# Kernel tuning notes

Hardware: AMD Instinct MI355X
Metric: run time of the kernel (lower is better)

Reference implementation:

```python
import jax, jax.numpy as jnp
import numpy as np

EMB = 128
BINS = 32
CUT = 5.0
NLAYER = 5
NHID = 4  # extra hidden linears in edge MLP (hidden_dim_list has 5 entries total)
N_NODES = 50000
N_EDGES = 800000
N_GRAPH = 256
NODE_CLASS = 100


def setup_inputs() -> dict:
    key = jax.random.key(0)
    ks = jax.random.split(key, 20)
    s = 0.02
    inp = {
        'z': jax.random.randint(ks[0], (N_NODES,), 0, NODE_CLASS),
        'pos': jax.random.normal(ks[1], (N_NODES, 3), dtype=jnp.float32) * 3.0,
        'batch': jnp.sort(jax.random.randint(ks[2], (N_NODES,), 0, N_GRAPH)),
        'edge_index': jax.random.randint(ks[3], (2, N_EDGES), 0, N_NODES),
        # parameters
        'atom_table': jax.random.normal(ks[4], (NODE_CLASS, EMB), dtype=jnp.float32) * s,
        'atom_w': jax.random.normal(ks[5], (EMB, EMB), dtype=jnp.float32) * s,
        'atom_b': jnp.zeros((EMB,), jnp.float32),
        'edge_emb_w': jax.random.normal(ks[6], (BINS, EMB), dtype=jnp.float32) * s,
        'edge_emb_b': jnp.zeros((EMB,), jnp.float32),
        'edge_w0': jax.random.normal(ks[7], (NLAYER, 3 * EMB, EMB), dtype=jnp.float32) * s,
        'edge_b0': jnp.zeros((NLAYER, EMB), jnp.float32),
        'edge_w': jax.random.normal(ks[8], (NLAYER, NHID, EMB, EMB), dtype=jnp.float32) * s,
        'edge_b': jnp.zeros((NLAYER, NHID, EMB), jnp.float32),
        'node_w': jax.random.normal(ks[9], (NLAYER, EMB, EMB), dtype=jnp.float32) * s,
        'node_b': jnp.zeros((NLAYER, EMB), jnp.float32),
        'out_w': jax.random.normal(ks[10], (EMB, 1), dtype=jnp.float32) * s,
        'out_b': jnp.zeros((1,), jnp.float32),
    }
    return inp


def reference(z, pos, batch, edge_index, atom_table, atom_w, atom_b,
              edge_emb_w, edge_emb_b, edge_w0, edge_b0, edge_w, edge_b,
              node_w, node_b, out_w, out_b):
    silu = jax.nn.silu
    row, col = edge_index[0], edge_index[1]

    # atom embedding + linear
    h_node = atom_table[z] @ atom_w + atom_b  # [N, EMB]

    # edge distances -> gaussian basis expansion (linear spacing, log_base=1.0)
    d = jnp.linalg.norm(pos[row] - pos[col], axis=-1)  # [E]
    mu = jnp.linspace(0.0, CUT, BINS, dtype=jnp.float32)
    sigma = CUT / BINS
    basis = jnp.exp(-0.5 * ((d[:, None] - mu) / sigma) ** 2)  # [E, BINS]
    h_edge = basis @ edge_emb_w + edge_emb_b  # [E, EMB]

    # message passing layers
    for l in range(NLAYER):
        m = jnp.concatenate([h_edge, h_node[row], h_node[col]], axis=-1)  # [E, 3*EMB]
        m = silu(m @ edge_w0[l] + edge_b0[l])
        for k in range(NHID):
            m = silu(m @ edge_w[l, k] + edge_b[l, k])
        h_edge = h_edge + m  # residual edge update
        agg = jax.ops.segment_sum(h_edge, row, num_segments=N_NODES)  # [N, EMB]
        h_node = h_node + silu(agg @ node_w[l] + node_b[l])  # residual node update

    # scatter-mean graph pool
    sums = jax.ops.segment_sum(h_node, batch, num_segments=N_GRAPH)
    cnt = jax.ops.segment_sum(jnp.ones((h_node.shape[0],), h_node.dtype), batch, num_segments=N_GRAPH)
    h_graph = sums / jnp.clip(cnt, 1.0)[:, None]

    return h_graph @ out_w + out_b  # [N_GRAPH, 1]
```

## Files before the change

### kernel.cpp

```cpp
#include <hip/hip_runtime.h>

#define EMB      128
#define N_NODES_ 50000
#define N_EDGES_ 800000
#define N_GRAPH_ 256
#define NLAYER_  5

#define WP_ATOM  573440
#define WP_NODE0 589824
#define WP_EMB   671744
#define WP_TOTAL 675840

typedef short short8 __attribute__((ext_vector_type(8)));
typedef float floatx4 __attribute__((ext_vector_type(4)));

__device__ __forceinline__ float silu_f(float x) {
    return __fdividef(x, 1.0f + __expf(-x));
}
__device__ __forceinline__ float bf2f(unsigned short h) {
    return __uint_as_float(((unsigned)h) << 16);
}
__device__ __forceinline__ unsigned short f2bf(float f) {
    unsigned u = __float_as_uint(f);
    unsigned r = 0x7FFFu + ((u >> 16) & 1u);
    return (unsigned short)((u + r) >> 16);
}

#if defined(__has_builtin)
#if __has_builtin(__builtin_amdgcn_cvt_pk_bf16_f32)
#define HAVE_PK_BF16 1
#endif
#endif
#ifdef HAVE_PK_BF16
typedef __bf16 bf16x2 __attribute__((ext_vector_type(2)));
__device__ __forceinline__ unsigned f2bf_pk(float a, float b) {
    bf16x2 v = __builtin_amdgcn_cvt_pk_bf16_f32(a, b);
    unsigned u;
    __builtin_memcpy(&u, &v, 4);
    return u;
}
#else
__device__ __forceinline__ unsigned f2bf_pk(float a, float b) {
    return (unsigned)f2bf(a) | ((unsigned)f2bf(b) << 16);
}
#endif

__device__ __forceinline__ void wave_lds_fence() {
    __builtin_amdgcn_fence(__ATOMIC_ACQ_REL, "wavefront");
    __builtin_amdgcn_wave_barrier();
}

__device__ __forceinline__ void gload_lds16(const unsigned short* g, unsigned short* l) {
    __builtin_amdgcn_global_load_lds(
        (const __attribute__((address_space(1))) void*)g,
        (__attribute__((address_space(3))) void*)l,
        16, 0, 0);
}

__global__ __launch_bounds__(256) void hist_kernel(
    const int* __restrict__ row, int* __restrict__ hist)
{
    const int e = blockIdx.x * 256 + threadIdx.x;
    if (e < N_EDGES_) atomicAdd(&hist[row[e]], 1);
}

__global__ __launch_bounds__(256) void scan_kernel(
    const int* __restrict__ hist, int* __restrict__ cursor)
{
    __shared__ int ssum[256];
    const int tid = threadIdx.x;
    const int chunk = (N_NODES_ + 255) / 256;
    const int base = tid * chunk;
    int s = 0;
    for (int i = 0; i < chunk; ++i) {
        const int idx = base + i;
        if (idx < N_NODES_) s += hist[idx];
    }
    ssum[tid] = s;
    __syncthreads();
    for (int off = 1; off < 256; off <<= 1) {
        const int t2 = (tid >= off) ? ssum[tid - off] : 0;
        __syncthreads();
        ssum[tid] += t2;
        __syncthreads();
    }
    int run = ssum[tid] - s;
    for (int i = 0; i < chunk; ++i) {
        const int idx = base + i;
        if (idx < N_NODES_) { cursor[idx] = run; run += hist[idx]; }
    }
}

__global__ __launch_bounds__(256) void scatter_kernel(
    const int* __restrict__ row, const int* __restrict__ col,
    int* __restrict__ cursor, int* __restrict__ row_s, int* __restrict__ col_s)
{
    const int e = blockIdx.x * 256 + threadIdx.x;
    if (e >= N_EDGES_) return;
    const int r = row[e];
    const int p = atomicAdd(&cursor[r], 1);
    row_s[p] = r;
    col_s[p] = col[e];
}

__global__ __launch_bounds__(256) void pack_w_kernel(
    const float* __restrict__ edge_w0, const float* __restrict__ edge_w,
    const float* __restrict__ atom_w, const float* __restrict__ node_w,
    const float* __restrict__ edge_emb_w,
    unsigned short* __restrict__ Wp)
{
    const int bid = blockIdx.x;
    int Kb, t;
    const float* src;
    unsigned short* dst;
    if (bid < 200) {
        const int l = bid / 40, r = bid % 40, s = r / 8;
        t = r % 8;
        Kb = (s == 0) ? 12 : 4;
        src = (s == 0) ? edge_w0 + (size_t)l * 384 * 128
                       : edge_w + ((size_t)l * 4 + (s - 1)) * 128 * 128;
        dst = Wp + (size_t)l * 114688 + ((s == 0) ? 0 : (49152 + (s - 1) * 16384))
            + (size_t)t * Kb * 512;
    } else if (bid < 208) {
        t = bid - 200; Kb = 4; src = atom_w;
        dst = Wp + WP_ATOM + (size_t)t * Kb * 512;
    } else if (bid < 248) {
        const int l = (bid - 208) >> 3; t = (bid - 208) & 7; Kb = 4;
        src = node_w + (size_t)l * 128 * 128;
        dst = Wp + WP_NODE0 + (size_t)l * 16384 + (size_t)t * Kb * 512;
    } else {
        t = bid - 248; Kb = 1; src = edge_emb_w;
        dst = Wp + WP_EMB + (size_t)t * 512;
    }
    const int n = Kb * 512;
    for (int p = threadIdx.x; p < n; p += 256) {
        const int j = p & 7, lane = (p >> 3) & 63, kb = p >> 9;
        const int k  = kb * 32 + ((lane >> 4) << 3) + j;
        const int nn = t * 16 + (lane & 15);
        dst[p] = f2bf(src[(size_t)k * 128 + nn]);
    }
}

__global__ __launch_bounds__(256, 4) void u_gemm_kernel(
    const unsigned short* __restrict__ h_node_bf,
    const unsigned short* __restrict__ Wp0, const float* __restrict__ b0,
    unsigned short* __restrict__ Ur, unsigned short* __restrict__ Uc, int N)
{
    __shared__ __align__(16) unsigned short B[64][136];
    const int tid  = threadIdx.x;
    const int lane = tid & 63;
    const int wv   = tid >> 6;
    const int n0   = blockIdx.x * 64;

    {
        const int t = tid >> 2, q = tid & 3;
        const int node = n0 + t;
#pragma unroll
        for (int i = 0; i < 4; ++i) {
            const int k8 = (q + 4 * i) << 3;
            short8 v = (short8){0,0,0,0,0,0,0,0};
            if (node < N) v = *(const short8*)&h_node_bf[(size_t)node * 128 + k8];
            *(short8*)&B[t][k8] = v;
        }
    }
    wave_lds_fence();

    const int lr = lane & 15, lg = lane >> 4;
    floatx4 accr[8], accc[8];
#pragma unroll
    for (int nt = 0; nt < 8; ++nt) {
        const float4 bv = *(const float4*)&b0[nt * 16 + lg * 4];
        accr[nt] = (floatx4){bv.x, bv.y, bv.z, bv.w};
        accc[nt] = (floatx4){0.f, 0.f, 0.f, 0.f};
    }
    const unsigned short* brow = &B[wv * 16 + lr][0];
#pragma unroll 2
    for (int kb = 0; kb < 4; ++kb) {
        const short8 mf = *(const short8*)(brow + kb * 32 + lg * 8);
#pragma unroll
        for (int nt = 0; nt < 8; ++nt) {
            const short8 wr = *(const short8*)(Wp0 + ((size_t)(nt * 12 + 4 + kb) * 64 + lane) * 8);
            const short8 wc = *(const short8*)(Wp0 + ((size_t)(nt * 12 + 8 + kb) * 64 + lane) * 8);
            accr[nt] = __builtin_amdgcn_mfma_f32_16x16x32_bf16(wr, mf, accr[nt], 0, 0, 0);
            accc[nt] = __builtin_amdgcn_mfma_f32_16x16x32_bf16(wc, mf, accc[nt], 0, 0, 0);
        }
    }
    const int node = n0 + wv * 16 + lr;
    if (node < N) {
        unsigned short* rrow = Ur + (size_t)node * 128;
        unsigned short* crow = Uc + (size_t)node * 128;
#pragma unroll
        for (int nt = 0; nt < 8; ++nt) {
            uint2 o;
            o.x = f2bf_pk(accr[nt][0], accr[nt][1]);
            o.y = f2bf_pk(accr[nt][2], accr[nt][3]);
            *(uint2*)(rrow + nt * 16 + lg * 4) = o;
            o.x = f2bf_pk(accc[nt][0], accc[nt][1]);
            o.y = f2bf_pk(accc[nt][2], accc[nt][3]);
            *(uint2*)(crow + nt * 16 + lg * 4) = o;
        }
    }
}

__global__ __launch_bounds__(256, 5) void edge_mlp_csr_kernel(
    const unsigned short* __restrict__ h_edge,
    const unsigned short* __restrict__ Ur, const unsigned short* __restrict__ Uc,
    const int* __restrict__ row_s, const int* __restrict__ col_s,
    const unsigned short* __restrict__ Wp, const float* __restrict__ bh)
{
    __shared__ __align__(16) unsigned short Xs[8192];
    __shared__ __align__(16) unsigned short Ys[8192];

    const int tid  = threadIdx.x;
    const int e0   = blockIdx.x * 64;
    const int lane = tid & 63;
    const int wv   = tid >> 6;
    const int lr   = lane & 15;
    const int lg   = lane >> 4;
    const int nt0  = 2 * wv, nt1 = nt0 + 1;

    int rid[4], cid[4];
#pragma unroll
    for (int et = 0; et < 4; ++et) {
        const int e = e0 + et * 16 + lr;
        rid[et] = row_s[e];
        cid[et] = col_s[e];
    }

    const int srow = 16 * wv + lg;
#pragma unroll
    for (int j = 0; j < 4; ++j) {
        const int r = srow + 4 * j;
        const int c = lr ^ (r & 7);
        gload_lds16(h_edge + (size_t)(e0 + r) * 128 + c * 8,
                    &Xs[(16 * wv + 4 * j) * 128]);
    }

    uint2 gr0[4], gr1[4], gc0[4], gc1[4];
#pragma unroll
    for (int et = 0; et < 4; ++et) {
        gr0[et] = *(const uint2*)(Ur + (size_t)rid[et] * 128 + nt0 * 16 + lg * 4);
        gr1[et] = *(const uint2*)(Ur + (size_t)rid[et] * 128 + nt1 * 16 + lg * 4);
        gc0[et] = *(const uint2*)(Uc + (size_t)cid[et] * 128 + nt0 * 16 + lg * 4);
        gc1[et] = *(const uint2*)(Uc + (size_t)cid[et] * 128 + nt1 * 16 + lg * 4);
    }

    asm volatile("s_waitcnt vmcnt(0)" ::: "memory");
    __syncthreads();

    floatx4 acc0[4], acc1[4];
#pragma unroll
    for (int et = 0; et < 4; ++et) {
        acc0[et][0] = bf2f((unsigned short)(gr0[et].x & 0xFFFF)) + bf2f((unsigned short)(gc0[et].x & 0xFFFF));
        acc0[et][1] = bf2f((unsigned short)(gr0[et].x >> 16))    + bf2f((unsigned short)(gc0[et].x >> 16));
        acc0[et][2] = bf2f((unsigned short)(gr0[et].y & 0xFFFF)) + bf2f((unsigned short)(gc0[et].y & 0xFFFF));
        acc0[et][3] = bf2f((unsigned short)(gr0[et].y >> 16))    + bf2f((unsigned short)(gc0[et].y >> 16));
        acc1[et][0] = bf2f((unsigned short)(gr1[et].x & 0xFFFF)) + bf2f((unsigned short)(gc1[et].x & 0xFFFF));
        acc1[et][1] = bf2f((unsigned short)(gr1[et].x >> 16))    + bf2f((unsigned short)(gc1[et].x >> 16));
        acc1[et][2] = bf2f((unsigned short)(gr1[et].y & 0xFFFF)) + bf2f((unsigned short)(gc1[et].y & 0xFFFF));
        acc1[et][3] = bf2f((unsigned short)(gr1[et].y >> 16))    + bf2f((unsigned short)(gc1[et].y >> 16));
    }

    const unsigned short* aptr0 = Wp + ((size_t)(nt0 * 12) * 64 + lane) * 8;
    const unsigned short* aptr1 = Wp + ((size_t)(nt1 * 12) * 64 + lane) * 8;
#pragma unroll 2
    for (int kk = 0; kk < 4; ++kk) {
        const short8 wf0 = *(const short8*)(aptr0 + (size_t)kk * 512);
        const short8 wf1 = *(const short8*)(aptr1 + (size_t)kk * 512);
#pragma unroll
        for (int et = 0; et < 4; ++et) {
            const int r = et * 16 + lr;
            const short8 mf = *(const short8*)&Xs[r * 128 + (((kk * 4 + lg) ^ (r & 7)) << 3)];
            acc0[et] = __builtin_amdgcn_mfma_f32_16x16x32_bf16(wf0, mf, acc0[et], 0, 0, 0);
            acc1[et] = __builtin_amdgcn_mfma_f32_16x16x32_bf16(wf1, mf, acc1[et], 0, 0, 0);
        }
    }

    const int t_ = tid >> 2, q_ = tid & 3;
    short8 he_reg[4];
#pragma unroll
    for (int i = 0; i < 4; ++i) {
        const int ch = q_ + 4 * i;
        he_reg[i] = *(const short8*)&Xs[t_ * 128 + ((ch ^ (t_ & 7)) << 3)];
    }

#pragma unroll
    for (int et = 0; et < 4; ++et) {
        const int r = et * 16 + lr;
        uint2 p0, p1;
        p0.x = f2bf_pk(silu_f(acc0[et][0]), silu_f(acc0[et][1]));
        p0.y = f2bf_pk(silu_f(acc0[et][2]), silu_f(acc0[et][3]));
        p1.x = f2bf_pk(silu_f(acc1[et][0]), silu_f(acc1[et][1]));
        p1.y = f2bf_pk(silu_f(acc1[et][2]), silu_f(acc1[et][3]));
        const int c0 = (2 * nt0 + (lg >> 1)) ^ (r & 7);
        const int c1 = (2 * nt1 + (lg >> 1)) ^ (r & 7);
        *(uint2*)&Ys[r * 128 + c0 * 8 + (lg & 1) * 4] = p0;
        *(uint2*)&Ys[r * 128 + c1 * 8 + (lg & 1) * 4] = p1;
    }
    __syncthreads();

#pragma unroll 1
    for (int s = 1; s < 5; ++s) {
        const unsigned short* bin = (s & 1) ? Ys : Xs;
        unsigned short* bout      = (s & 1) ? Xs : Ys;
        const unsigned short* __restrict__ Ws = Wp + 49152 + (size_t)(s - 1) * 16384;
        const float* __restrict__ bias = bh + (size_t)(s - 1) * 128;

        const float4 bv0 = *(const float4*)&bias[nt0 * 16 + lg * 4];
        const float4 bv1 = *(const float4*)&bias[nt1 * 16 + lg * 4];
#pragma unroll
        for (int et = 0; et < 4; ++et) {
            acc0[et] = (floatx4){bv0.x, bv0.y, bv0.z, bv0.w};
            acc1[et] = (floatx4){bv1.x, bv1.y, bv1.z, bv1.w};
        }
        const unsigned short* ap0 = Ws + ((size_t)(nt0 * 4) * 64 + lane) * 8;
        const unsigned short* ap1 = Ws + ((size_t)(nt1 * 4) * 64 + lane) * 8;
#pragma unroll 2
        for (int kk = 0; kk < 4; ++kk) {
            const short8 wf0 = *(const short8*)(ap0 + (size_t)kk * 512);
            const short8 wf1 = *(const short8*)(ap1 + (size_t)kk * 512);
#pragma unroll
            for (int et = 0; et < 4; ++et) {
                const int r = et * 16 + lr;
                const short8 mf = *(const short8*)&bin[r * 128 + (((kk * 4 + lg) ^ (r & 7)) << 3)];
                acc0[et] = __builtin_amdgcn_mfma_f32_16x16x32_bf16(wf0, mf, acc0[et], 0, 0, 0);
                acc1[et] = __builtin_amdgcn_mfma_f32_16x16x32_bf16(wf1, mf, acc1[et], 0, 0, 0);
            }
        }
#pragma unroll
        for (int et = 0; et < 4; ++et) {
            const int r = et * 16 + lr;
            uint2 p0, p1;
            p0.x = f2bf_pk(silu_f(acc0[et][0]), silu_f(acc0[et][1]));
            p0.y = f2bf_pk(silu_f(acc0[et][2]), silu_f(acc0[et][3]));
            p1.x = f2bf_pk(silu_f(acc1[et][0]), silu_f(acc1[et][1]));
            p1.y = f2bf_pk(silu_f(acc1[et][2]), silu_f(acc1[et][3]));
            const int c0 = (2 * nt0 + (lg >> 1)) ^ (r & 7);
            const int c1 = (2 * nt1 + (lg >> 1)) ^ (r & 7);
            *(uint2*)&bout[r * 128 + c0 * 8 + (lg & 1) * 4] = p0;
            *(uint2*)&bout[r * 128 + c1 * 8 + (lg & 1) * 4] = p1;
        }
        __syncthreads();
    }

#pragma unroll
    for (int i = 0; i < 4; ++i) {
        const int ch = q_ + 4 * i;
        const short8 mv = *(const short8*)&Ys[t_ * 128 + ((ch ^ (t_ & 7)) << 3)];
        const short8 ov = he_reg[i];
        float he[8];
#pragma unroll
        for (int j = 0; j < 8; ++j)
            he[j] = bf2f((unsigned short)ov[j]) + bf2f((unsigned short)mv[j]);
        uint4 sv;
        sv.x = f2bf_pk(he[0], he[1]);
        sv.y = f2bf_pk(he[2], he[3]);
        sv.z = f2bf_pk(he[4], he[5]);
        sv.w = f2bf_pk(he[6], he[7]);
        *(uint4*)(const_cast<unsigned short*>(h_edge) + (size_t)(e0 + t_) * 128 + ch * 8) = sv;
    }
}

__global__ __launch_bounds__(256, 4) void node_agg_gemm_kernel(
    const unsigned short* __restrict__ h_edge,
    const int* __restrict__ hist, const int* __restrict__ cur_end,
    const unsigned short* __restrict__ Wpm, const float* __restrict__ bias,
    unsigned short* __restrict__ h_node_bf, int N)
{
    __shared__ __align__(16) unsigned short B[64][136];
    const int tid  = threadIdx.x;
    const int lane = tid & 63;
    const int wv   = tid >> 6;
    const int n0   = blockIdx.x * 64;

    {
        const int t = tid >> 2, q = tid & 3;
        const int n = n0 + t;
        float a[32];
#pragma unroll
        for (int j = 0; j < 32; ++j) a[j] = 0.f;
        if (n < N) {
            const int e_end = cur_end[n];
            const int e_beg = e_end - hist[n];
            for (int e = e_beg; e < e_end; ++e) {
                const unsigned short* p = &h_edge[(size_t)e * 128 + q * 32];
#pragma unroll
                for (int g = 0; g < 4; ++g) {
                    const short8 v = *(const short8*)(p + g * 8);
#pragma unroll
                    for (int j = 0; j < 8; ++j)
                        a[g * 8 + j] += bf2f((unsigned short)v[j]);
                }
            }
        }
#pragma unroll
        for (int g = 0; g < 4; ++g) {
            uint4 pk;
            pk.x = f2bf_pk(a[g * 8 + 0], a[g * 8 + 1]);
            pk.y = f2bf_pk(a[g * 8 + 2], a[g * 8 + 3]);
            pk.z = f2bf_pk(a[g * 8 + 4], a[g * 8 + 5]);
            pk.w = f2bf_pk(a[g * 8 + 6], a[g * 8 + 7]);
            *(uint4*)&B[t][q * 32 + g * 8] = pk;
        }
    }
    wave_lds_fence();

    const int lr = lane & 15, lg = lane >> 4;
    floatx4 acc[8];
#pragma unroll
    for (int nt = 0; nt < 8; ++nt) {
        const float4 bv = *(const float4*)&bias[nt * 16 + lg * 4];
        acc[nt] = (floatx4){bv.x, bv.y, bv.z, bv.w};
    }
    const unsigned short* brow = &B[wv * 16 + lr][0];
#pragma unroll 2
    for (int kb = 0; kb < 4; ++kb) {
        const short8 mf = *(const short8*)(brow + kb * 32 + lg * 8);
#pragma unroll
        for (int nt = 0; nt < 8; ++nt) {
            const short8 wf = *(const short8*)(Wpm + ((size_t)(nt * 4 + kb) * 64 + lane) * 8);
            acc[nt] = __builtin_amdgcn_mfma_f32_16x16x32_bf16(wf, mf, acc[nt], 0, 0, 0);
        }
    }
    const int node = n0 + wv * 16 + lr;
    if (node < N) {
        unsigned short* drow = &h_node_bf[(size_t)node * 128];
#pragma unroll
        for (int nt = 0; nt < 8; ++nt) {
            float x0 = silu_f(acc[nt][0]), x1 = silu_f(acc[nt][1]);
            float x2 = silu_f(acc[nt][2]), x3 = silu_f(acc[nt][3]);
            unsigned short* p = drow + nt * 16 + lg * 4;
            const uint2 d = *(const uint2*)p;
            x0 += bf2f((unsigned short)(d.x & 0xFFFF));
            x1 += bf2f((unsigned short)(d.x >> 16));
            x2 += bf2f((unsigned short)(d.y & 0xFFFF));
            x3 += bf2f((unsigned short)(d.y >> 16));
            uint2 o;
            o.x = f2bf_pk(x0, x1);
            o.y = f2bf_pk(x2, x3);
            *(uint2*)p = o;
        }
    }
}

__global__ __launch_bounds__(256, 4) void atom_gemm_mfma_kernel(
    const float* __restrict__ src, const int* __restrict__ gidx,
    const unsigned short* __restrict__ Wpm, const float* __restrict__ bias,
    unsigned short* __restrict__ dst, int N)
{
    __shared__ __align__(16) unsigned short B[64][136];
    const int tid  = threadIdx.x;
    const int lane = tid & 63;
    const int wv   = tid >> 6;
    const int n0   = blockIdx.x * 64;

    {
        const int t = tid >> 2, q = tid & 3;
        const int node = n0 + t;
        const float* srow = src;
        if (node < N) srow = &src[(size_t)gidx[node] * 128];
#pragma unroll
        for (int i = 0; i < 4; ++i) {
            const int k8 = (q + 4 * i) << 3;
            uint4 pk = make_uint4(0, 0, 0, 0);
            if (node < N) {
                const float4 f0 = *(const float4*)(srow + k8);
                const float4 f1 = *(const float4*)(srow + k8 + 4);
                pk.x = f2bf_pk(f0.x, f0.y);
                pk.y = f2bf_pk(f0.z, f0.w);
                pk.z = f2bf_pk(f1.x, f1.y);
                pk.w = f2bf_pk(f1.z, f1.w);
            }
            *(uint4*)&B[t][k8] = pk;
        }
    }
    wave_lds_fence();

    const int lr = lane & 15, lg = lane >> 4;
    floatx4 acc[8];
#pragma unroll
    for (int nt = 0; nt < 8; ++nt) {
        const float4 bv = *(const float4*)&bias[nt * 16 + lg * 4];
        acc[nt] = (floatx4){bv.x, bv.y, bv.z, bv.w};
    }
    const unsigned short* brow = &B[wv * 16 + lr][0];
#pragma unroll 2
    for (int kb = 0; kb < 4; ++kb) {
        const short8 mf = *(const short8*)(brow + kb * 32 + lg * 8);
#pragma unroll
        for (int nt = 0; nt < 8; ++nt) {
            const short8 wf = *(const short8*)(Wpm + ((size_t)(nt * 4 + kb) * 64 + lane) * 8);
            acc[nt] = __builtin_amdgcn_mfma_f32_16x16x32_bf16(wf, mf, acc[nt], 0, 0, 0);
        }
    }
    const int node = n0 + wv * 16 + lr;
    if (node < N) {
        unsigned short* drow = &dst[(size_t)node * 128];
#pragma unroll
        for (int nt = 0; nt < 8; ++nt) {
            uint2 o;
            o.x = f2bf_pk(acc[nt][0], acc[nt][1]);
            o.y = f2bf_pk(acc[nt][2], acc[nt][3]);
            *(uint2*)(drow + nt * 16 + lg * 4) = o;
        }
    }
}

__global__ __launch_bounds__(256, 4) void edge_embed_mfma_kernel(
    const float* __restrict__ pos, const int* __restrict__ row, const int* __restrict__ col,
    const unsigned short* __restrict__ Wpe, const float* __restrict__ bemb,
    unsigned short* __restrict__ h_edge)
{
    __shared__ __align__(16) unsigned short Bas[64][40];
    const int tid  = threadIdx.x;
    const int lane = tid & 63;
    const int wv   = tid >> 6;
    const int e0   = blockIdx.x * 64;

    {
        const int t = tid >> 2, q = tid & 3;
        const int rr = row[e0 + t], cc = col[e0 + t];
        const float dx = pos[rr * 3 + 0] - pos[cc * 3 + 0];
        const float dy = pos[rr * 3 + 1] - pos[cc * 3 + 1];
        const float dz = pos[rr * 3 + 2] - pos[cc * 3 + 2];
        const float d = sqrtf(dx * dx + dy * dy + dz * dz);
        const float invs = 32.0f / 5.0f;
        float e[8];
#pragma unroll
        for (int j = 0; j < 8; ++j) {
            const float mu = (float)(q * 8 + j) * (5.0f / 31.0f);
            const float tt = (d - mu) * invs;
            e[j] = __expf(-0.5f * tt * tt);
        }
        uint4 pk;
        pk.x = f2bf_pk(e[0], e[1]);
        pk.y = f2bf_pk(e[2], e[3]);
        pk.z = f2bf_pk(e[4], e[5]);
        pk.w = f2bf_pk(e[6], e[7]);
        *(uint4*)&Bas[t][q * 8] = pk;
    }
    wave_lds_fence();

    const int lr = lane & 15, lg = lane >> 4;
    floatx4 acc[8];
#pragma unroll
    for (int nt = 0; nt < 8; ++nt) {
        const float4 bv = *(const float4*)&bemb[nt * 16 + lg * 4];
        acc[nt] = (floatx4){bv.x, bv.y, bv.z, bv.w};
    }
    const short8 mf = *(const short8*)&Bas[wv * 16 + lr][lg * 8];
#pragma unroll
    for (int nt = 0; nt < 8; ++nt) {
        const short8 wf = *(const short8*)(Wpe + ((size_t)nt * 64 + lane) * 8);
        acc[nt] = __builtin_amdgcn_mfma_f32_16x16x32_bf16(wf, mf, acc[nt], 0, 0, 0);
    }
    unsigned short* erow = &h_edge[(size_t)(e0 + wv * 16 + lr) * 128];
#pragma unroll
    for (int nt = 0; nt < 8; ++nt) {
        uint2 o;
        o.x = f2bf_pk(acc[nt][0], acc[nt][1]);
        o.y = f2bf_pk(acc[nt][2], acc[nt][3]);
        *(uint2*)(erow + nt * 16 + lg * 4) = o;
    }
}

__global__ __launch_bounds__(128) void pool_kernel(
    const unsigned short* __restrict__ h_node_bf, const int* __restrict__ batch,
    float* __restrict__ sums, float* __restrict__ cnt, int N)
{
    __shared__ int bb[256];
    const int tid = threadIdx.x;
    const int n0 = blockIdx.x * 256;
    for (int idx = tid; idx < 256; idx += 128) {
        int n = n0 + idx;
        bb[idx] = (n < N) ? batch[n] : -1;
    }
    __syncthreads();
    int cur = bb[0];
    float run = 0.f, runc = 0.f;
    for (int i = 0; i < 256; ++i) {
        const int b = bb[i];
        if (b < 0) break;
        if (b != cur) {
            atomicAdd(&sums[(size_t)cur * 128 + tid], run);
            if (tid == 0) atomicAdd(&cnt[cur], runc);
            run = 0.f; runc = 0.f; cur = b;
        }
        run += bf2f(h_node_bf[(size_t)(n0 + i) * 128 + tid]);
        runc += 1.f;
    }
    atomicAdd(&sums[(size_t)cur * 128 + tid], run);
    if (tid == 0) atomicAdd(&cnt[cur], runc);
}

__global__ __launch_bounds__(256) void final_kernel(
    const float* __restrict__ sums, const float* __restrict__ cnt,
    const float* __restrict__ out_w, const float* __restrict__ out_b,
    float* __restrict__ out)
{
    const int g = threadIdx.x;
    const float c = fmaxf(cnt[g], 1.0f);
    float acc = 0.f;
    for (int jj = 0; jj < 128; ++jj) acc = fmaf(sums[(size_t)g * 128 + jj], out_w[jj], acc);
    out[g] = acc / c + out_b[0];
}

__global__ void zero_out_kernel(float* out, int n) {
    int i = blockIdx.x * 256 + threadIdx.x;
    if (i < n) out[i] = 0.f;
}


extern "C" void kernel_launch(void* const* d_in, const int* in_sizes, int n_in,
                              void* d_out, int out_size, void* d_ws, size_t ws_size,
                              hipStream_t stream)
{
    const int*   z          = (const int*)  d_in[0];
    const float* pos        = (const float*)d_in[1];
    const int*   batch      = (const int*)  d_in[2];
    const int*   eidx       = (const int*)  d_in[3];
    const float* atom_table = (const float*)d_in[4];
    const float* atom_w     = (const float*)d_in[5];
    const float* atom_b     = (const float*)d_in[6];
    const float* edge_emb_w = (const float*)d_in[7];
    const float* edge_emb_b = (const float*)d_in[8];
    const float* edge_w0    = (const float*)d_in[9];
    const float* edge_b0    = (const float*)d_in[10];
    const float* edge_w     = (const float*)d_in[11];
    const float* edge_b     = (const float*)d_in[12];
    const float* node_w     = (const float*)d_in[13];
    const float* node_b     = (const float*)d_in[14];
    const float* out_w      = (const float*)d_in[15];
    const float* out_b      = (const float*)d_in[16];
    const int* row = eidx;
    const int* col = eidx + N_EDGES_;

    float* aggb = (float*)d_ws;
    float* sums = aggb + (size_t)N_NODES_ * EMB;
    float* cnt  = sums + (size_t)N_GRAPH_ * EMB;
    unsigned short* h_node_bf = (unsigned short*)(cnt + N_GRAPH_);
    unsigned short* h_edge    = h_node_bf + (size_t)N_NODES_ * EMB;
    unsigned short* Wp        = h_edge + (size_t)N_EDGES_ * EMB;
    int* hist   = (int*)(Wp + WP_TOTAL);
    int* cursor = hist + N_NODES_;
    int* row_s  = cursor + N_NODES_;
    int* col_s  = row_s + N_EDGES_;

    unsigned short* Ur = (unsigned short*)aggb;
    unsigned short* Uc = Ur + (size_t)N_NODES_ * EMB;

    const size_t need = ((size_t)(N_NODES_ * EMB + N_GRAPH_ * EMB + N_GRAPH_)) * 4
                      + ((size_t)N_NODES_ * EMB + (size_t)N_EDGES_ * EMB + (size_t)WP_TOTAL) * 2
                      + ((size_t)N_NODES_ * 2 + (size_t)N_EDGES_ * 2) * 4;

    if (ws_size < need) {
        zero_out_kernel<<<1, 256, 0, stream>>>((float*)d_out, N_GRAPH_);
        return;
    }

    const int grid_rows64 = (N_NODES_ + 63) / 64;

    (void)hipMemsetAsync(hist, 0, N_NODES_ * sizeof(int), stream);
    hist_kernel<<<(N_EDGES_ + 255) / 256, 256, 0, stream>>>(row, hist);
    scan_kernel<<<1, 256, 0, stream>>>(hist, cursor);
    scatter_kernel<<<(N_EDGES_ + 255) / 256, 256, 0, stream>>>(row, col, cursor, row_s, col_s);

    pack_w_kernel<<<256, 256, 0, stream>>>(edge_w0, edge_w, atom_w, node_w, edge_emb_w, Wp);

    atom_gemm_mfma_kernel<<<grid_rows64, 256, 0, stream>>>(
        atom_table, z, Wp + WP_ATOM, atom_b, h_node_bf, N_NODES_);
    edge_embed_mfma_kernel<<<N_EDGES_ / 64, 256, 0, stream>>>(
        pos, row_s, col_s, Wp + WP_EMB, edge_emb_b, h_edge);

    for (int l = 0; l < NLAYER_; ++l) {
        u_gemm_kernel<<<grid_rows64, 256, 0, stream>>>(
            h_node_bf, Wp + (size_t)l * 114688, edge_b0 + (size_t)l * 128,
            Ur, Uc, N_NODES_);
        edge_mlp_csr_kernel<<<N_EDGES_ / 64, 256, 0, stream>>>(
            h_edge, Ur, Uc, row_s, col_s,
            Wp + (size_t)l * 114688,
            edge_b + (size_t)l * 4 * 128);
        node_agg_gemm_kernel<<<grid_rows64, 256, 0, stream>>>(
            h_edge, hist, cursor,
            Wp + WP_NODE0 + (size_t)l * 16384, node_b + (size_t)l * 128,
            h_node_bf, N_NODES_);
    }

    (void)hipMemsetAsync(sums, 0, ((size_t)N_GRAPH_ * EMB + N_GRAPH_) * sizeof(float), stream);
    pool_kernel<<<(N_NODES_ + 255) / 256, 128, 0, stream>>>(h_node_bf, batch, sums, cnt, N_NODES_);
    final_kernel<<<1, 256, 0, stream>>>(sums, cnt, out_w, out_b, (float*)d_out);
}
```

Baseline: 2.532 ms.

## Keep edge MLP activations in registers using permlane swaps instead of LDS

Result: slower. 3.646 ms (+44.0%).

```diff
diff --git a/kernel.cpp b/kernel.cpp
--- a/kernel.cpp
+++ b/kernel.cpp
@@ -13,6 +13,7 @@
 
 typedef short short8 __attribute__((ext_vector_type(8)));
 typedef float floatx4 __attribute__((ext_vector_type(4)));
+typedef unsigned uintx2 __attribute__((ext_vector_type(2)));
 
 __device__ __forceinline__ float silu_f(float x) {
     return __fdividef(x, 1.0f + __expf(-x));
@@ -30,7 +31,11 @@
 #if __has_builtin(__builtin_amdgcn_cvt_pk_bf16_f32)
 #define HAVE_PK_BF16 1
 #endif
+#if __has_builtin(__builtin_amdgcn_permlane16_swap) && __has_builtin(__builtin_amdgcn_permlane32_swap)
+#define HAVE_PERMLANE_SWAP 1
 #endif
+#endif
+
 #ifdef HAVE_PK_BF16
 typedef __bf16 bf16x2 __attribute__((ext_vector_type(2)));
 __device__ __forceinline__ unsigned f2bf_pk(float a, float b) {
@@ -50,11 +55,52 @@
     __builtin_amdgcn_wave_barrier();
 }
 
-__device__ __forceinline__ void gload_lds16(const unsigned short* g, unsigned short* l) {
-    __builtin_amdgcn_global_load_lds(
-        (const __attribute__((address_space(1))) void*)g,
-        (__attribute__((address_space(3))) void*)l,
-        16, 0, 0);
+__device__ __forceinline__ void swap32(unsigned &a, unsigned &b) {
+#ifdef HAVE_PERMLANE_SWAP
+    uintx2 r = __builtin_amdgcn_permlane32_swap(a, b, false, false);
+    a = r.x; b = r.y;
+#else
+    const int lane = (int)(threadIdx.x & 63);
+    const int idx = (lane ^ 32) << 2;
+    const unsigned ta = (unsigned)__builtin_amdgcn_ds_bpermute(idx, (int)a);
+    const unsigned tb = (unsigned)__builtin_amdgcn_ds_bpermute(idx, (int)b);
+    const bool hi = lane >= 32;
+    const unsigned na = hi ? tb : a;
+    const unsigned nb = hi ? b : ta;
+    a = na; b = nb;
+#endif
+}
+__device__ __forceinline__ void swap16(unsigned &a, unsigned &b) {
+#ifdef HAVE_PERMLANE_SWAP
+    uintx2 r = __builtin_amdgcn_permlane16_swap(a, b, false, false);
+    a = r.x; b = r.y;
+#else
+    const unsigned ta = (unsigned)__builtin_amdgcn_ds_swizzle((int)a, 0x401F);
+    const unsigned tb = (unsigned)__builtin_amdgcn_ds_swizzle((int)b, 0x401F);
+    const bool odd = ((threadIdx.x >> 4) & 1) != 0;
+    const unsigned na = odd ? tb : a;
+    const unsigned nb = odd ? b : ta;
+    a = na; b = nb;
+#endif
+}
+
+__device__ __forceinline__ short8 xchg_frag(uint2 pkE, uint2 pkO) {
+    unsigned a0 = pkE.x, b0 = pkO.x;
+    unsigned a1 = pkE.y, b1 = pkO.y;
+    swap32(a0, b0); swap16(a0, b0);
+    swap32(a1, b1); swap16(a1, b1);
+    union { short8 s; unsigned u[4]; } r;
+    r.u[0] = a0; r.u[1] = a1; r.u[2] = b0; r.u[3] = b1;
+    return r.s;
+}
+
+__device__ __forceinline__ floatx4 upair_sum(uint2 a, uint2 b) {
+    floatx4 r;
+    r[0] = bf2f((unsigned short)(a.x & 0xFFFF)) + bf2f((unsigned short)(b.x & 0xFFFF));
+    r[1] = bf2f((unsigned short)(a.x >> 16))    + bf2f((unsigned short)(b.x >> 16));
+    r[2] = bf2f((unsigned short)(a.y & 0xFFFF)) + bf2f((unsigned short)(b.y & 0xFFFF));
+    r[3] = bf2f((unsigned short)(a.y >> 16))    + bf2f((unsigned short)(b.y >> 16));
+    return r;
 }
 
 __global__ __launch_bounds__(256) void hist_kernel(
@@ -202,162 +248,98 @@
     }
 }
 
-__global__ __launch_bounds__(256, 5) void edge_mlp_csr_kernel(
-    const unsigned short* __restrict__ h_edge,
+__global__ __launch_bounds__(256, 3) void edge_mlp_csr_kernel(
+    unsigned short* __restrict__ h_edge,
     const unsigned short* __restrict__ Ur, const unsigned short* __restrict__ Uc,
     const int* __restrict__ row_s, const int* __restrict__ col_s,
     const unsigned short* __restrict__ Wp, const float* __restrict__ bh)
 {
-    __shared__ __align__(16) unsigned short Xs[8192];
-    __shared__ __align__(16) unsigned short Ys[8192];
-
     const int tid  = threadIdx.x;
-    const int e0   = blockIdx.x * 64;
     const int lane = tid & 63;
-    const int wv   = tid >> 6;
     const int lr   = lane & 15;
     const int lg   = lane >> 4;
-    const int nt0  = 2 * wv, nt1 = nt0 + 1;
-
-    int rid[4], cid[4];
-#pragma unroll
-    for (int et = 0; et < 4; ++et) {
-        const int e = e0 + et * 16 + lr;
-        rid[et] = row_s[e];
-        cid[et] = col_s[e];
-    }
-
-    const int srow = 16 * wv + lg;
-#pragma unroll
-    for (int j = 0; j < 4; ++j) {
-        const int r = srow + 4 * j;
-        const int c = lr ^ (r & 7);
-        gload_lds16(h_edge + (size_t)(e0 + r) * 128 + c * 8,
-                    &Xs[(16 * wv + 4 * j) * 128]);
-    }
-
-    uint2 gr0[4], gr1[4], gc0[4], gc1[4];
-#pragma unroll
-    for (int et = 0; et < 4; ++et) {
-        gr0[et] = *(const uint2*)(Ur + (size_t)rid[et] * 128 + nt0 * 16 + lg * 4);
-        gr1[et] = *(const uint2*)(Ur + (size_t)rid[et] * 128 + nt1 * 16 + lg * 4);
-        gc0[et] = *(const uint2*)(Uc + (size_t)cid[et] * 128 + nt0 * 16 + lg * 4);
-        gc1[et] = *(const uint2*)(Uc + (size_t)cid[et] * 128 + nt1 * 16 + lg * 4);
-    }
-
-    asm volatile("s_waitcnt vmcnt(0)" ::: "memory");
-    __syncthreads();
-
-    floatx4 acc0[4], acc1[4];
-#pragma unroll
-    for (int et = 0; et < 4; ++et) {
-        acc0[et][0] = bf2f((unsigned short)(gr0[et].x & 0xFFFF)) + bf2f((unsigned short)(gc0[et].x & 0xFFFF));
-        acc0[et][1] = bf2f((unsigned short)(gr0[et].x >> 16))    + bf2f((unsigned short)(gc0[et].x >> 16));
-        acc0[et][2] = bf2f((unsigned short)(gr0[et].y & 0xFFFF)) + bf2f((unsigned short)(gc0[et].y & 0xFFFF));
-        acc0[et][3] = bf2f((unsigned short)(gr0[et].y >> 16))    + bf2f((unsigned short)(gc0[et].y >> 16));
-        acc1[et][0] = bf2f((unsigned short)(gr1[et].x & 0xFFFF)) + bf2f((unsigned short)(gc1[et].x & 0xFFFF));
-        acc1[et][1] = bf2f((unsigned short)(gr1[et].x >> 16))    + bf2f((unsigned short)(gc1[et].x >> 16));
-        acc1[et][2] = bf2f((unsigned short)(gr1[et].y & 0xFFFF)) + bf2f((unsigned short)(gc1[et].y & 0xFFFF));
-        acc1[et][3] = bf2f((unsigned short)(gr1[et].y >> 16))    + bf2f((unsigned short)(gc1[et].y >> 16));
-    }
-
-    const unsigned short* aptr0 = Wp + ((size_t)(nt0 * 12) * 64 + lane) * 8;
-    const unsigned short* aptr1 = Wp + ((size_t)(nt1 * 12) * 64 + lane) * 8;
-#pragma unroll 2
-    for (int kk = 0; kk < 4; ++kk) {
-        const short8 wf0 = *(const short8*)(aptr0 + (size_t)kk * 512);
-        const short8 wf1 = *(const short8*)(aptr1 + (size_t)kk * 512);
-#pragma unroll
-        for (int et = 0; et < 4; ++et) {
-            const int r = et * 16 + lr;
-            const short8 mf = *(const short8*)&Xs[r * 128 + (((kk * 4 + lg) ^ (r & 7)) << 3)];
-            acc0[et] = __builtin_amdgcn_mfma_f32_16x16x32_bf16(wf0, mf, acc0[et], 0, 0, 0);
-            acc1[et] = __builtin_amdgcn_mfma_f32_16x16x32_bf16(wf1, mf, acc1[et], 0, 0, 0);
-        }
-    }
-
-    const int t_ = tid >> 2, q_ = tid & 3;
-    short8 he_reg[4];
-#pragma unroll
-    for (int i = 0; i < 4; ++i) {
-        const int ch = q_ + 4 * i;
-        he_reg[i] = *(const short8*)&Xs[t_ * 128 + ((ch ^ (t_ & 7)) << 3)];
-    }
-
-#pragma unroll
-    for (int et = 0; et < 4; ++et) {
-        const int r = et * 16 + lr;
-        uint2 p0, p1;
-        p0.x = f2bf_pk(silu_f(acc0[et][0]), silu_f(acc0[et][1]));
-        p0.y = f2bf_pk(silu_f(acc0[et][2]), silu_f(acc0[et][3]));
-        p1.x = f2bf_pk(silu_f(acc1[et][0]), silu_f(acc1[et][1]));
-        p1.y = f2bf_pk(silu_f(acc1[et][2]), silu_f(acc1[et][3]));
-        const int c0 = (2 * nt0 + (lg >> 1)) ^ (r & 7);
-        const int c1 = (2 * nt1 + (lg >> 1)) ^ (r & 7);
-        *(uint2*)&Ys[r * 128 + c0 * 8 + (lg & 1) * 4] = p0;
-        *(uint2*)&Ys[r * 128 + c1 * 8 + (lg & 1) * 4] = p1;
-    }
-    __syncthreads();
-
-#pragma unroll 1
-    for (int s = 1; s < 5; ++s) {
-        const unsigned short* bin = (s & 1) ? Ys : Xs;
-        unsigned short* bout      = (s & 1) ? Xs : Ys;
-        const unsigned short* __restrict__ Ws = Wp + 49152 + (size_t)(s - 1) * 16384;
-        const float* __restrict__ bias = bh + (size_t)(s - 1) * 128;
-
-        const float4 bv0 = *(const float4*)&bias[nt0 * 16 + lg * 4];
-        const float4 bv1 = *(const float4*)&bias[nt1 * 16 + lg * 4];
-#pragma unroll
-        for (int et = 0; et < 4; ++et) {
-            acc0[et] = (floatx4){bv0.x, bv0.y, bv0.z, bv0.w};
-            acc1[et] = (floatx4){bv1.x, bv1.y, bv1.z, bv1.w};
-        }
-        const unsigned short* ap0 = Ws + ((size_t)(nt0 * 4) * 64 + lane) * 8;
-        const unsigned short* ap1 = Ws + ((size_t)(nt1 * 4) * 64 + lane) * 8;
-#pragma unroll 2
-        for (int kk = 0; kk < 4; ++kk) {
-            const short8 wf0 = *(const short8*)(ap0 + (size_t)kk * 512);
-            const short8 wf1 = *(const short8*)(ap1 + (size_t)kk * 512);
-#pragma unroll
-            for (int et = 0; et < 4; ++et) {
-                const int r = et * 16 + lr;
-                const short8 mf = *(const short8*)&bin[r * 128 + (((kk * 4 + lg) ^ (r & 7)) << 3)];
-                acc0[et] = __builtin_amdgcn_mfma_f32_16x16x32_bf16(wf0, mf, acc0[et], 0, 0, 0);
-                acc1[et] = __builtin_amdgcn_mfma_f32_16x16x32_bf16(wf1, mf, acc1[et], 0, 0, 0);
+    const int e0   = blockIdx.x * 128 + (tid >> 6) * 32;
+
+    const int eA = e0 + lr, eB = eA + 16;
+    const int ridA = row_s[eA], cidA = col_s[eA];
+    const int ridB = row_s[eB], cidB = col_s[eB];
+
+    short8 bf[2][4];
+#pragma unroll
+    for (int kb = 0; kb < 4; ++kb) {
+        bf[0][kb] = *(const short8*)&h_edge[(size_t)eA * 128 + kb * 32 + lg * 8];
+        bf[1][kb] = *(const short8*)&h_edge[(size_t)eB * 128 + kb * 32 + lg * 8];
+    }
+
+    floatx4 acc[2][8];
+#pragma unroll
+    for (int nt = 0; nt < 8; ++nt) {
+        const int fo = nt * 16 + lg * 4;
+        const uint2 rA = *(const uint2*)(Ur + (size_t)ridA * 128 + fo);
+        const uint2 cA = *(const uint2*)(Uc + (size_t)cidA * 128 + fo);
+        const uint2 rB = *(const uint2*)(Ur + (size_t)ridB * 128 + fo);
+        const uint2 cB = *(const uint2*)(Uc + (size_t)cidB * 128 + fo);
+        acc[0][nt] = upair_sum(rA, cA);
+        acc[1][nt] = upair_sum(rB, cB);
+    }
+
+#pragma unroll
+    for (int s = 0; s < 5; ++s) {
+        const unsigned short* __restrict__ Ws =
+            (s == 0) ? Wp : (Wp + 49152 + (size_t)(s - 1) * 16384);
+        const int nst = (s == 0) ? 12 : 4;
+#pragma unroll
+        for (int nt = 0; nt < 8; ++nt) {
+#pragma unroll
+            for (int kb = 0; kb < 4; ++kb) {
+                const short8 wf = *(const short8*)(Ws + ((size_t)(nt * nst + kb) * 64 + lane) * 8);
+                acc[0][nt] = __builtin_amdgcn_mfma_f32_16x16x32_bf16(wf, bf[0][kb], acc[0][nt], 0, 0, 0);
+                acc[1][nt] = __builtin_amdgcn_mfma_f32_16x16x32_bf16(wf, bf[1][kb], acc[1][nt], 0, 0, 0);
             }
         }
-#pragma unroll
-        for (int et = 0; et < 4; ++et) {
-            const int r = et * 16 + lr;
-            uint2 p0, p1;
-            p0.x = f2bf_pk(silu_f(acc0[et][0]), silu_f(acc0[et][1]));
-            p0.y = f2bf_pk(silu_f(acc0[et][2]), silu_f(acc0[et][3]));
-            p1.x = f2bf_pk(silu_f(acc1[et][0]), silu_f(acc1[et][1]));
-            p1.y = f2bf_pk(silu_f(acc1[et][2]), silu_f(acc1[et][3]));
-            const int c0 = (2 * nt0 + (lg >> 1)) ^ (r & 7);
-            const int c1 = (2 * nt1 + (lg >> 1)) ^ (r & 7);
-            *(uint2*)&bout[r * 128 + c0 * 8 + (lg & 1) * 4] = p0;
-            *(uint2*)&bout[r * 128 + c1 * 8 + (lg & 1) * 4] = p1;
-        }
-        __syncthreads();
-    }
-
-#pragma unroll
-    for (int i = 0; i < 4; ++i) {
-        const int ch = q_ + 4 * i;
-        const short8 mv = *(const short8*)&Ys[t_ * 128 + ((ch ^ (t_ & 7)) << 3)];
-        const short8 ov = he_reg[i];
-        float he[8];
-#pragma unroll
-        for (int j = 0; j < 8; ++j)
-            he[j] = bf2f((unsigned short)ov[j]) + bf2f((unsigned short)mv[j]);
-        uint4 sv;
-        sv.x = f2bf_pk(he[0], he[1]);
-        sv.y = f2bf_pk(he[2], he[3]);
-        sv.z = f2bf_pk(he[4], he[5]);
-        sv.w = f2bf_pk(he[6], he[7]);
-        *(uint4*)(const_cast<unsigned short*>(h_edge) + (size_t)(e0 + t_) * 128 + ch * 8) = sv;
+        uint2 pk[2][8];
+#pragma unroll
+        for (int h = 0; h < 2; ++h)
+#pragma unroll
+            for (int nt = 0; nt < 8; ++nt) {
+                pk[h][nt].x = f2bf_pk(silu_f(acc[h][nt][0]), silu_f(acc[h][nt][1]));
+                pk[h][nt].y = f2bf_pk(silu_f(acc[h][nt][2]), silu_f(acc[h][nt][3]));
+            }
+#pragma unroll
+        for (int h = 0; h < 2; ++h)
+#pragma unroll
+            for (int kb = 0; kb < 4; ++kb)
+                bf[h][kb] = xchg_frag(pk[h][2 * kb], pk[h][2 * kb + 1]);
+
+        if (s < 4) {
+            const float* bias = bh + s * 128;
+#pragma unroll
+            for (int nt = 0; nt < 8; ++nt) {
+                const float4 bv = *(const float4*)&bias[nt * 16 + lg * 4];
+                acc[0][nt] = (floatx4){bv.x, bv.y, bv.z, bv.w};
+                acc[1][nt] = acc[0][nt];
+            }
+        }
+    }
+
+#pragma unroll
+    for (int h = 0; h < 2; ++h) {
+        unsigned short* erow = h_edge + (size_t)((h == 0) ? eA : eB) * 128 + lg * 8;
+#pragma unroll
+        for (int kb = 0; kb < 4; ++kb) {
+            const short8 ov = *(const short8*)(erow + kb * 32);
+            const short8 mv = bf[h][kb];
+            float v[8];
+#pragma unroll
+            for (int j = 0; j < 8; ++j)
+                v[j] = bf2f((unsigned short)ov[j]) + bf2f((unsigned short)mv[j]);
+            uint4 sv;
+            sv.x = f2bf_pk(v[0], v[1]);
+            sv.y = f2bf_pk(v[2], v[3]);
+            sv.z = f2bf_pk(v[4], v[5]);
+            sv.w = f2bf_pk(v[6], v[7]);
+            *(uint4*)(erow + kb * 32) = sv;
+        }
     }
 }
 
@@ -676,7 +658,7 @@
         u_gemm_kernel<<<grid_rows64, 256, 0, stream>>>(
             h_node_bf, Wp + (size_t)l * 114688, edge_b0 + (size_t)l * 128,
             Ur, Uc, N_NODES_);
-        edge_mlp_csr_kernel<<<N_EDGES_ / 64, 256, 0, stream>>>(
+        edge_mlp_csr_kernel<<<N_EDGES_ / 128, 256, 0, stream>>>(
             h_edge, Ur, Uc, row_s, col_s,
             Wp + (size_t)l * 114688,
             edge_b + (size_t)l * 4 * 128);
```
